# Kernel tuning notes

Measured on AMD Instinct MI355X. Metric: run time of the kernel, lower is better.

Reference implementation:

```python
import jax, jax.numpy as jnp
import numpy as np
from jax import lax

B, N0, N1 = 4, 256, 256
NVOX = N0 * N1
NSUB, NLOR, RAYLEN, NTOF = 8, 32768, 256, 1
NBLK, CH = 4, 16
SUBSETS = np.linspace(0, NSUB, NBLK, endpoint=False).astype(int)  # [0,2,4,6]


def setup_inputs() -> dict:
    key = jax.random.key(0)
    ks = jax.random.split(key, 12)
    osem = jax.random.uniform(ks[0], (B, 1, N0, N1, 1), jnp.float32) + 0.1
    data = jax.random.uniform(ks[1], (B, NSUB, NLOR, NTOF), jnp.float32)
    mult = jax.random.uniform(ks[2], (B, NSUB, NLOR, 1), jnp.float32) + 0.5
    contam = jax.random.uniform(ks[3], (B, NSUB, NLOR, NTOF), jnp.float32) + 0.1
    adjoint_ones = jax.random.uniform(ks[4], (B, NSUB, N0, N1, 1), jnp.float32) + 0.5
    norm = jax.random.uniform(ks[5], (B,), jnp.float32) + 0.5
    ray_idx = jax.random.randint(ks[6], (NSUB, NLOR, RAYLEN), 0, NVOX, dtype=jnp.int32)
    proj_weights = jax.random.uniform(ks[7], (NSUB, NLOR, RAYLEN), jnp.float32) / RAYLEN
    w1 = jax.random.normal(ks[8], (CH, 1, 3, 3), jnp.float32) * 0.05
    b1 = jnp.zeros((CH,), jnp.float32)
    w2 = jax.random.normal(ks[9], (1, CH, 3, 3), jnp.float32) * 0.05
    b2 = jnp.zeros((1,), jnp.float32)
    net_weight = jnp.asarray(1.0, jnp.float32)
    return dict(osem=osem, data=data, multiplicative_corrections=mult,
                contamination=contam, adjoint_ones=adjoint_ones, norm=norm,
                ray_idx=ray_idx, proj_weights=proj_weights,
                w1=w1, b1=b1, w2=w2, b2=b2, net_weight=net_weight)


def _conv(x, w):
    return lax.conv_general_dilated(x, w, (1, 1), 'SAME',
                                    dimension_numbers=('NCHW', 'OIHW', 'NCHW'))


def _net(x, w1, b1, w2, b2):
    # x: (B,1,N0,N1,1) -> treat as NCHW 2D image with 1 channel
    img = x[:, :, :, :, 0]
    h = jax.nn.relu(_conv(img, w1) + b1[None, :, None, None])
    o = _conv(h, w2) + b2[None, :, None, None]
    return o[..., None]


def _fidelity(x, data, mult, contam, adj_ones, norm, ray_idx, pw, subset):
    # unscaled image, flattened: (B, NVOX)
    img_flat = norm[:, None] * x[:, 0, :, :, 0].reshape(B, NVOX)
    ii = ray_idx[subset]          # (NLOR, RAYLEN) voxel indices per ray
    ww = pw[subset]               # (NLOR, RAYLEN) Joseph weights
    # forward projection: gather + weighted sum along each ray
    fwd = jnp.einsum('bls,ls->bl', img_flat[:, ii], ww)[..., None]  # (B,NLOR,1)
    expected = mult[:, subset] * fwd + contam[:, subset]            # (B,NLOR,NTOF)
    ratio = (mult[:, subset] * (1.0 - data[:, subset] / expected)).sum(-1)  # (B,NLOR)
    # adjoint projection: scatter-add along each ray
    back = jnp.zeros((B, NVOX), x.dtype).at[:, ii].add(ww * ratio[:, :, None])
    upd = back * (img_flat / adj_ones[:, subset].reshape(B, NVOX))
    return (upd / norm[:, None]).reshape(B, 1, N0, N1, 1)


def reference(osem, data, multiplicative_corrections, contamination,
              adjoint_ones, norm, ray_idx, proj_weights,
              w1, b1, w2, b2, net_weight):
    x = osem
    for subset in SUBSETS:
        x_data = _fidelity(x, data, multiplicative_corrections, contamination,
                           adjoint_ones, norm, ray_idx, proj_weights, int(subset))
        x_net = _net(x, w1, b1, w2, b2)
        x = jax.nn.relu(osem - x_data + net_weight * x_net)
    return x
```

## Files before the change

kernel.cpp:

```cpp
#include <hip/hip_runtime.h>
#include <hip/hip_fp16.h>

#define BB 4
#define N0 256
#define N1 256
#define NVOX 65536
#define NSUB 8
#define NLOR 32768
#define RAYLEN 256
#define CH 16
#define NPTS (NLOR * RAYLEN)
#define VOXQ 16384
#define VOXT 32768
#define CCH 32

__global__ __launch_bounds__(256) void k_transpose(const float* __restrict__ osem,
                                                   float* __restrict__ xt) {
    int v = blockIdx.x * blockDim.x + threadIdx.x;
    if (v >= NVOX) return;
    float4 o;
    o.x = osem[0 * NVOX + v];
    o.y = osem[1 * NVOX + v];
    o.z = osem[2 * NVOX + v];
    o.w = osem[3 * NVOX + v];
    ((float4*)xt)[v] = o;
}

__device__ __forceinline__ float upk_w(unsigned p) {
    return __half2float(__ushort_as_half((unsigned short)(p >> 16)));
}

__device__ __forceinline__ unsigned pk2(float a, float b) {
    __half2 h = __floats2half2_rn(a, b);
    return *reinterpret_cast<unsigned*>(&h);
}

__global__ __launch_bounds__(256) void k_fwdpack(
    const int* __restrict__ ridx,
    const float* __restrict__ pw,
    const float* __restrict__ xt,
    const float* __restrict__ data,
    const float* __restrict__ mult,
    const float* __restrict__ contam,
    const float* __restrict__ norm,
    float* __restrict__ ratio,
    unsigned* __restrict__ packed)
{
    const int wave = threadIdx.x >> 6;
    const int lane = threadIdx.x & 63;
    const int l = blockIdx.x * 4 + wave;
    const long e = (long)l * 64 + lane;

    int4   id = ((const int4*)ridx)[e];
    float4 w  = ((const float4*)pw)[e];
    uint4 pk;
    pk.x = (unsigned)id.x | ((unsigned)__half_as_ushort(__float2half_rn(w.x)) << 16);
    pk.y = (unsigned)id.y | ((unsigned)__half_as_ushort(__float2half_rn(w.y)) << 16);
    pk.z = (unsigned)id.z | ((unsigned)__half_as_ushort(__float2half_rn(w.z)) << 16);
    pk.w = (unsigned)id.w | ((unsigned)__half_as_ushort(__float2half_rn(w.w)) << 16);
    ((uint4*)packed)[e] = pk;

    float ax = 0.f, ay = 0.f, az = 0.f, aw = 0.f;
    {
        float4 xv = ((const float4*)xt)[id.x];
        ax += xv.x * w.x; ay += xv.y * w.x; az += xv.z * w.x; aw += xv.w * w.x;
        xv = ((const float4*)xt)[id.y];
        ax += xv.x * w.y; ay += xv.y * w.y; az += xv.z * w.y; aw += xv.w * w.y;
        xv = ((const float4*)xt)[id.z];
        ax += xv.x * w.z; ay += xv.y * w.z; az += xv.z * w.z; aw += xv.w * w.z;
        xv = ((const float4*)xt)[id.w];
        ax += xv.x * w.w; ay += xv.y * w.w; az += xv.z * w.w; aw += xv.w * w.w;
    }
#pragma unroll
    for (int off = 32; off >= 1; off >>= 1) {
        ax += __shfl_xor(ax, off);
        ay += __shfl_xor(ay, off);
        az += __shfl_xor(az, off);
        aw += __shfl_xor(aw, off);
    }
    if (lane == 0) {
        float fwd[4] = {ax, ay, az, aw};
        float rr[4];
#pragma unroll
        for (int b = 0; b < 4; ++b) {
            long o = (long)b * (NSUB * NLOR) + l;
            float m = mult[o];
            float ee = m * (norm[b] * fwd[b]) + contam[o];
            rr[b] = m * (1.0f - data[o] / ee);
        }
        ((float4*)ratio)[l] = make_float4(rr[0], rr[1], rr[2], rr[3]);
    }
}

__global__ __launch_bounds__(1024) void k_back_pk(
    const unsigned* __restrict__ packed,
    const float* __restrict__ ratio,
    unsigned* __restrict__ part,
    int PC)
{
    __shared__ unsigned acc[VOXQ];
    const int c = blockIdx.x;
    const int g = blockIdx.y;
    const int p = g & 1;
    const unsigned lo = (unsigned)(g >> 1) * VOXQ;

    for (int q = threadIdx.x; q < VOXQ; q += 1024) acc[q] = 0u;
    __syncthreads();

    const unsigned abase = (unsigned)(uintptr_t)(&acc[0]);

    const int n4 = PC >> 2;
    const uint4* src = (const uint4*)packed + (size_t)c * n4;
    const float2* rat2 = (const float2*)ratio;
    const int e0 = c * n4;

#define PKADD(u, R)                                                              \
    {                                                                            \
        unsigned q_ = ((u) & 0xffffu) - lo;                                      \
        if (q_ < VOXQ) {                                                         \
            float w_ = upk_w(u);                                                 \
            unsigned d_ = pk2(w_ * (R).x, w_ * (R).y);                           \
            unsigned a_ = abase + (q_ << 2);                                     \
            asm volatile("ds_pk_add_f16 %0, %1" :: "v"(a_), "v"(d_) : "memory"); \
        }                                                                        \
    }
#define PROC(P, R) PKADD(P.x, R) PKADD(P.y, R) PKADD(P.z, R) PKADD(P.w, R)

    for (int base4 = 0; base4 < n4; base4 += 4096) {
        const int ea = base4 + (int)threadIdx.x;
        uint4 A = src[ea];
        uint4 B = src[ea + 1024];
        uint4 C2 = src[ea + 2048];
        uint4 D = src[ea + 3072];
        float2 ra = rat2[(((e0 + ea) >> 6) << 1) + p];
        float2 rb = rat2[(((e0 + ea + 1024) >> 6) << 1) + p];
        float2 rc = rat2[(((e0 + ea + 2048) >> 6) << 1) + p];
        float2 rd = rat2[(((e0 + ea + 3072) >> 6) << 1) + p];
        PROC(A, ra) PROC(B, rb) PROC(C2, rc) PROC(D, rd)
    }
#undef PROC
#undef PKADD

    asm volatile("s_waitcnt lgkmcnt(0)" ::: "memory");
    __syncthreads();

    unsigned* dst = part + ((size_t)c * 2 + p) * NVOX + lo;
    for (int q = threadIdx.x; q < VOXQ; q += 1024) dst[q] = acc[q];
}

__global__ __launch_bounds__(256) void k_reduce(
    const unsigned* __restrict__ part,
    float* __restrict__ back)
{
    const int v = blockIdx.x * 256 + threadIdx.x;
    const int pr = blockIdx.y;
    float s0 = 0.f, s1 = 0.f;
#pragma unroll 8
    for (int cc = 0; cc < CCH; ++cc) {
        unsigned u = part[((size_t)cc * 2 + pr) * NVOX + v];
        s0 += __half2float(__ushort_as_half((unsigned short)(u & 0xffffu)));
        s1 += __half2float(__ushort_as_half((unsigned short)(u >> 16)));
    }
    ((float2*)back)[(size_t)v * 2 + pr] = make_float2(s0, s1);
}

#define TI 16
#define TJ 32
__global__ __launch_bounds__(256) void k_net_combine(
    const float* __restrict__ xt_in,
    const float* __restrict__ w1,
    const float* __restrict__ b1,
    const float* __restrict__ w2,
    const float* __restrict__ b2,
    const float* __restrict__ back,
    const float* __restrict__ osem,
    const float* __restrict__ adj,
    const float* __restrict__ nwp,
    float* __restrict__ xt_out,
    float* __restrict__ out_planar)
{
    __shared__ float img[(TI + 4) * (TJ + 4)];
    __shared__ float hsm[16 * (TI + 2) * (TJ + 2)];
    __shared__ float ws1[144], ws2[144], bs1[16];

    const int i0 = blockIdx.x * TI;
    const int j0 = blockIdx.y * TJ;
    const int b  = blockIdx.z;
    const int tid = threadIdx.x;

    if (tid < 144) { ws1[tid] = w1[tid]; ws2[tid] = w2[tid]; }
    if (tid < 16) bs1[tid] = b1[tid];

    for (int q = tid; q < (TI + 4) * (TJ + 4); q += 256) {
        int ii = q / (TJ + 4), jj = q % (TJ + 4);
        int gi = i0 - 2 + ii, gj = j0 - 2 + jj;
        float v = 0.f;
        if (gi >= 0 && gi < N0 && gj >= 0 && gj < N1)
            v = xt_in[(size_t)(gi * N1 + gj) * 4 + b];
        img[q] = v;
    }
    __syncthreads();

    const int HA = (TI + 2) * (TJ + 2);
    for (int q = tid; q < 16 * HA; q += 256) {
        int c = q / HA, r = q % HA;
        int ii = r / (TJ + 2), jj = r % (TJ + 2);
        int gi = i0 - 1 + ii, gj = j0 - 1 + jj;
        float hv = 0.f;
        if (gi >= 0 && gi < N0 && gj >= 0 && gj < N1) {
            float a = bs1[c];
#pragma unroll
            for (int di = 0; di < 3; ++di)
#pragma unroll
                for (int dj = 0; dj < 3; ++dj)
                    a += img[(ii + di) * (TJ + 4) + (jj + dj)] * ws1[c * 9 + di * 3 + dj];
            hv = fmaxf(a, 0.f);
        }
        hsm[q] = hv;
    }
    __syncthreads();

    const float nw = nwp[0];
    const float bb2 = b2[0];
    const int pr = b >> 1, hi = b & 1;
    for (int q = tid; q < TI * TJ; q += 256) {
        int li = q / TJ, lj = q % TJ;
        int v = (i0 + li) * N1 + (j0 + lj);
        float o = bb2;
#pragma unroll
        for (int c = 0; c < 16; ++c)
#pragma unroll
            for (int di = 0; di < 3; ++di)
#pragma unroll
                for (int dj = 0; dj < 3; ++dj)
                    o += hsm[c * HA + (li + di) * (TJ + 2) + (lj + dj)] *
                         ws2[c * 9 + di * 3 + dj];
        float2 bp = ((const float2*)back)[(size_t)v * 2 + pr];
        float bk = hi ? bp.y : bp.x;
        float xv = xt_in[(size_t)v * 4 + b];
        float x_data = bk * xv / adj[(size_t)b * NSUB * NVOX + v];
        float xnew = fmaxf(osem[(size_t)b * NVOX + v] - x_data + nw * o, 0.f);
        xt_out[(size_t)v * 4 + b] = xnew;
        if (out_planar) out_planar[(size_t)b * NVOX + v] = xnew;
    }
}

__global__ __launch_bounds__(256) void k_fwd(
    const int* __restrict__ ridx, const float* __restrict__ pw,
    const float* __restrict__ xt, const float* __restrict__ data,
    const float* __restrict__ mult, const float* __restrict__ contam,
    const float* __restrict__ norm, float* __restrict__ ratio)
{
    const int wave = threadIdx.x >> 6;
    const int lane = threadIdx.x & 63;
    const int l = blockIdx.x * 4 + wave;
    const long base = (long)l * RAYLEN;
    float ax = 0.f, ay = 0.f, az = 0.f, aw = 0.f;
#pragma unroll
    for (int k = 0; k < 4; ++k) {
        int r = lane + (k << 6);
        float wt = pw[base + r];
        float4 xv = ((const float4*)xt)[ridx[base + r]];
        ax += xv.x * wt; ay += xv.y * wt; az += xv.z * wt; aw += xv.w * wt;
    }
#pragma unroll
    for (int off = 32; off >= 1; off >>= 1) {
        ax += __shfl_xor(ax, off); ay += __shfl_xor(ay, off);
        az += __shfl_xor(az, off); aw += __shfl_xor(aw, off);
    }
    if (lane == 0) {
        float fwd[4] = {ax, ay, az, aw};
        float rr[4];
#pragma unroll
        for (int b = 0; b < 4; ++b) {
            long o = (long)b * (NSUB * NLOR) + l;
            float m = mult[o];
            float e = m * (norm[b] * fwd[b]) + contam[o];
            rr[b] = m * (1.0f - data[o] / e);
        }
        ((float4*)ratio)[l] = make_float4(rr[0], rr[1], rr[2], rr[3]);
    }
}

__global__ __launch_bounds__(1024) void k_back(
    const int* __restrict__ ridx, const float* __restrict__ pw,
    const float* __restrict__ ratio, float* __restrict__ part, int PC)
{
    __shared__ float acc[VOXT];
    const int c = blockIdx.x;
    const int g = blockIdx.y;
    const int b = g & 3;
    const int lo = (g >> 2) * VOXT;
    for (int q = threadIdx.x; q < VOXT; q += 1024) acc[q] = 0.0f;
    __syncthreads();
    const int pbeg = c * PC;
    const int pend = min(pbeg + PC, NPTS);
#pragma unroll 2
    for (int pt = pbeg + (int)threadIdx.x * 4; pt < pend; pt += 1024 * 4) {
        int4   id = *(const int4*)(ridx + pt);
        float4 w  = *(const float4*)(pw + pt);
        float  r  = ratio[(pt >> 8) * 4 + b];
        unsigned r0 = (unsigned)(id.x - lo), r1 = (unsigned)(id.y - lo);
        unsigned r2 = (unsigned)(id.z - lo), r3 = (unsigned)(id.w - lo);
        if (r0 < VOXT) atomicAdd(&acc[r0], w.x * r);
        if (r1 < VOXT) atomicAdd(&acc[r1], w.y * r);
        if (r2 < VOXT) atomicAdd(&acc[r2], w.z * r);
        if (r3 < VOXT) atomicAdd(&acc[r3], w.w * r);
    }
    __syncthreads();
    float4* dst = (float4*)(part + ((size_t)c * 4 + b) * NVOX + lo);
    const float4* srcl = (const float4*)acc;
    for (int q = threadIdx.x; q < VOXT / 4; q += 1024) dst[q] = srcl[q];
}

__global__ __launch_bounds__(256) void k_conv1(
    const float* __restrict__ xt, const float* __restrict__ w1,
    const float* __restrict__ b1, float* __restrict__ h)
{
    int t = blockIdx.x * blockDim.x + threadIdx.x;
    int b = t >> 16;
    int v = t & 65535;
    int i = v >> 8, j = v & 255;
    float in[3][3];
#pragma unroll
    for (int di = 0; di < 3; ++di)
#pragma unroll
        for (int dj = 0; dj < 3; ++dj) {
            int ii = i + di - 1, jj = j + dj - 1;
            in[di][dj] = (ii >= 0 && ii < N0 && jj >= 0 && jj < N1)
                             ? xt[(size_t)((ii << 8) | jj) * 4 + b]
                             : 0.0f;
        }
    float* hp = h + (size_t)t * CH;
#pragma unroll
    for (int c = 0; c < CH; ++c) {
        float acc = b1[c];
#pragma unroll
        for (int di = 0; di < 3; ++di)
#pragma unroll
            for (int dj = 0; dj < 3; ++dj)
                acc += in[di][dj] * w1[c * 9 + di * 3 + dj];
        hp[c] = fmaxf(acc, 0.0f);
    }
}

__global__ __launch_bounds__(256) void k_combine(
    const float* __restrict__ h, const float* __restrict__ w2,
    const float* __restrict__ b2, const float* __restrict__ part,
    const float* __restrict__ xt_in, const float* __restrict__ osem,
    const float* __restrict__ adj, const float* __restrict__ nwp, int C,
    float* __restrict__ xt_out, float* __restrict__ out_planar)
{
    int t = blockIdx.x * blockDim.x + threadIdx.x;
    int b = t >> 16;
    int v = t & 65535;
    int i = v >> 8, j = v & 255;
    float o = b2[0];
#pragma unroll
    for (int di = 0; di < 3; ++di) {
        int ii = i + di - 1;
        if (ii < 0 || ii >= N0) continue;
#pragma unroll
        for (int dj = 0; dj < 3; ++dj) {
            int jj = j + dj - 1;
            if (jj < 0 || jj >= N1) continue;
            const float* hp = h + ((size_t)b * NVOX + ((ii << 8) | jj)) * CH;
#pragma unroll
            for (int c = 0; c < CH; ++c)
                o += hp[c] * w2[c * 9 + di * 3 + dj];
        }
    }
    float bk = 0.0f;
    for (int c = 0; c < C; ++c)
        bk += part[((size_t)c * 4 + b) * NVOX + v];
    float xv = xt_in[(size_t)v * 4 + b];
    float x_data = bk * xv / adj[(size_t)b * NSUB * NVOX + v];
    float xnew = osem[t] - x_data + nwp[0] * o;
    xnew = fmaxf(xnew, 0.0f);
    xt_out[(size_t)v * 4 + b] = xnew;
    if (out_planar) out_planar[t] = xnew;
}

extern "C" void kernel_launch(void* const* d_in, const int* in_sizes, int n_in,
                              void* d_out, int out_size, void* d_ws, size_t ws_size,
                              hipStream_t stream) {
    const float* osem   = (const float*)d_in[0];
    const float* data   = (const float*)d_in[1];
    const float* mult   = (const float*)d_in[2];
    const float* contam = (const float*)d_in[3];
    const float* adj    = (const float*)d_in[4];
    const float* norm   = (const float*)d_in[5];
    const int*   ray_idx = (const int*)d_in[6];
    const float* pw     = (const float*)d_in[7];
    const float* w1     = (const float*)d_in[8];
    const float* b1     = (const float*)d_in[9];
    const float* w2     = (const float*)d_in[10];
    const float* b2     = (const float*)d_in[11];
    const float* nw     = (const float*)d_in[12];
    float* out = (float*)d_out;

    const size_t MB = 1024 * 1024;
    float* ws  = (float*)d_ws;
    float* xtA = ws;
    float* xtB = ws + (size_t)NVOX * 4;
    const int subsets[4] = {0, 2, 4, 6};

    bool use_pk = (ws_size >= 90 * MB);

    k_transpose<<<NVOX / 256, 256, 0, stream>>>(osem, xtA);

    if (use_pk) {
        const int PC = NPTS / CCH;
        unsigned* part   = (unsigned*)(ws + (size_t)NVOX * 8);
        unsigned* packed = part + (size_t)CCH * 2 * NVOX;
        float*    backv  = (float*)(packed + (size_t)NPTS);
        float*    ratio  = backv + (size_t)NVOX * 4;

        float* xin = xtA;
        float* xout = xtB;
        for (int it = 0; it < 4; ++it) {
            int s = subsets[it];
            k_fwdpack<<<NLOR / 4, 256, 0, stream>>>(
                ray_idx + (size_t)s * NPTS, pw + (size_t)s * NPTS, xin,
                data + (size_t)s * NLOR, mult + (size_t)s * NLOR,
                contam + (size_t)s * NLOR, norm, ratio, packed);
            k_back_pk<<<dim3(CCH, 8), 1024, 0, stream>>>(packed, ratio, part, PC);
            k_reduce<<<dim3(NVOX / 256, 2), 256, 0, stream>>>(part, backv);
            k_net_combine<<<dim3(N0 / TI, N1 / TJ, BB), 256, 0, stream>>>(
                xin, w1, b1, w2, b2, backv, osem,
                adj + (size_t)s * NVOX, nw,
                xout, (it == 3) ? out : nullptr);
            float* tmp = xin; xin = xout; xout = tmp;
        }
    } else {
        int C = (ws_size >= (18 + 32) * MB + NVOX) ? 32
              : (ws_size >= (18 + 16) * MB + NVOX) ? 16 : 8;
        const int PC = NPTS / C;
        float* part = ws + (size_t)NVOX * 8;
        float* h    = part + (size_t)C * NVOX * 4;
        float* ratio = h;

        float* xin = xtA;
        float* xout = xtB;
        for (int it = 0; it < 4; ++it) {
            int s = subsets[it];
            const int*   rs = ray_idx + (size_t)s * NPTS;
            const float* ps = pw + (size_t)s * NPTS;
            k_fwd<<<NLOR / 4, 256, 0, stream>>>(
                rs, ps, xin,
                data + (size_t)s * NLOR, mult + (size_t)s * NLOR,
                contam + (size_t)s * NLOR, norm, ratio);
            k_back<<<dim3(C, 8), 1024, 0, stream>>>(rs, ps, ratio, part, PC);
            k_conv1<<<(BB * NVOX) / 256, 256, 0, stream>>>(xin, w1, b1, h);
            k_combine<<<(BB * NVOX) / 256, 256, 0, stream>>>(
                h, w2, b2, part, xin, osem,
                adj + (size_t)s * NVOX, nw, C,
                xout, (it == 3) ? out : nullptr);
            float* tmp = xin; xin = xout; xout = tmp;
        }
    }
}
```

Before: 667.7 us.

## Split rays across half-waves, vectorize partial reduction, retile net conv into channel passes

The forward-pack kernel now has each half-wave handle one ray with eight gathers per lane, which halves the shuffle-reduction depth and the number of blocks. The reduce kernel reads two packed half2 words per thread so loads are wider. The conv/combine kernel uses 8-row tiles and computes the hidden channels in two passes of 8, which halves the hidden-layer shared memory. Each thread now owns exactly one output pixel and takes the center value from the shared image tile instead of reloading it. The changes target occupancy and instruction overhead, at the cost of an extra barrier and more halo recomputation per tile.

```diff
diff --git a/kernel.cpp b/kernel.cpp
--- a/kernel.cpp
+++ b/kernel.cpp
@@ -48,37 +48,59 @@
 {
     const int wave = threadIdx.x >> 6;
     const int lane = threadIdx.x & 63;
-    const int l = blockIdx.x * 4 + wave;
-    const long e = (long)l * 64 + lane;
-
-    int4   id = ((const int4*)ridx)[e];
-    float4 w  = ((const float4*)pw)[e];
-    uint4 pk;
-    pk.x = (unsigned)id.x | ((unsigned)__half_as_ushort(__float2half_rn(w.x)) << 16);
-    pk.y = (unsigned)id.y | ((unsigned)__half_as_ushort(__float2half_rn(w.y)) << 16);
-    pk.z = (unsigned)id.z | ((unsigned)__half_as_ushort(__float2half_rn(w.z)) << 16);
-    pk.w = (unsigned)id.w | ((unsigned)__half_as_ushort(__float2half_rn(w.w)) << 16);
-    ((uint4*)packed)[e] = pk;
+    const int half = lane >> 5;
+    const int sub  = lane & 31;
+    const int l = blockIdx.x * 8 + wave * 2 + half;
+    const long e0 = (long)l * 64;
+
+    const long ea = e0 + sub;
+    const long eb = e0 + sub + 32;
+
+    int4   ida = ((const int4*)ridx)[ea];
+    float4 wa  = ((const float4*)pw)[ea];
+    int4   idb = ((const int4*)ridx)[eb];
+    float4 wb  = ((const float4*)pw)[eb];
+
+    uint4 pka, pkb;
+    pka.x = (unsigned)ida.x | ((unsigned)__half_as_ushort(__float2half_rn(wa.x)) << 16);
+    pka.y = (unsigned)ida.y | ((unsigned)__half_as_ushort(__float2half_rn(wa.y)) << 16);
+    pka.z = (unsigned)ida.z | ((unsigned)__half_as_ushort(__float2half_rn(wa.z)) << 16);
+    pka.w = (unsigned)ida.w | ((unsigned)__half_as_ushort(__float2half_rn(wa.w)) << 16);
+    pkb.x = (unsigned)idb.x | ((unsigned)__half_as_ushort(__float2half_rn(wb.x)) << 16);
+    pkb.y = (unsigned)idb.y | ((unsigned)__half_as_ushort(__float2half_rn(wb.y)) << 16);
+    pkb.z = (unsigned)idb.z | ((unsigned)__half_as_ushort(__float2half_rn(wb.z)) << 16);
+    pkb.w = (unsigned)idb.w | ((unsigned)__half_as_ushort(__float2half_rn(wb.w)) << 16);
+    ((uint4*)packed)[ea] = pka;
+    ((uint4*)packed)[eb] = pkb;
 
     float ax = 0.f, ay = 0.f, az = 0.f, aw = 0.f;
     {
-        float4 xv = ((const float4*)xt)[id.x];
-        ax += xv.x * w.x; ay += xv.y * w.x; az += xv.z * w.x; aw += xv.w * w.x;
-        xv = ((const float4*)xt)[id.y];
-        ax += xv.x * w.y; ay += xv.y * w.y; az += xv.z * w.y; aw += xv.w * w.y;
-        xv = ((const float4*)xt)[id.z];
-        ax += xv.x * w.z; ay += xv.y * w.z; az += xv.z * w.z; aw += xv.w * w.z;
-        xv = ((const float4*)xt)[id.w];
-        ax += xv.x * w.w; ay += xv.y * w.w; az += xv.z * w.w; aw += xv.w * w.w;
-    }
-#pragma unroll
-    for (int off = 32; off >= 1; off >>= 1) {
+        float4 xv;
+        xv = ((const float4*)xt)[ida.x];
+        ax += xv.x * wa.x; ay += xv.y * wa.x; az += xv.z * wa.x; aw += xv.w * wa.x;
+        xv = ((const float4*)xt)[ida.y];
+        ax += xv.x * wa.y; ay += xv.y * wa.y; az += xv.z * wa.y; aw += xv.w * wa.y;
+        xv = ((const float4*)xt)[ida.z];
+        ax += xv.x * wa.z; ay += xv.y * wa.z; az += xv.z * wa.z; aw += xv.w * wa.z;
+        xv = ((const float4*)xt)[ida.w];
+        ax += xv.x * wa.w; ay += xv.y * wa.w; az += xv.z * wa.w; aw += xv.w * wa.w;
+        xv = ((const float4*)xt)[idb.x];
+        ax += xv.x * wb.x; ay += xv.y * wb.x; az += xv.z * wb.x; aw += xv.w * wb.x;
+        xv = ((const float4*)xt)[idb.y];
+        ax += xv.x * wb.y; ay += xv.y * wb.y; az += xv.z * wb.y; aw += xv.w * wb.y;
+        xv = ((const float4*)xt)[idb.z];
+        ax += xv.x * wb.z; ay += xv.y * wb.z; az += xv.z * wb.z; aw += xv.w * wb.z;
+        xv = ((const float4*)xt)[idb.w];
+        ax += xv.x * wb.w; ay += xv.y * wb.w; az += xv.z * wb.w; aw += xv.w * wb.w;
+    }
+#pragma unroll
+    for (int off = 16; off >= 1; off >>= 1) {
         ax += __shfl_xor(ax, off);
         ay += __shfl_xor(ay, off);
         az += __shfl_xor(az, off);
         aw += __shfl_xor(aw, off);
     }
-    if (lane == 0) {
+    if (sub == 0) {
         float fwd[4] = {ax, ay, az, aw};
         float rr[4];
 #pragma unroll
@@ -152,19 +174,23 @@
     const unsigned* __restrict__ part,
     float* __restrict__ back)
 {
-    const int v = blockIdx.x * 256 + threadIdx.x;
+    const int t = blockIdx.x * 256 + threadIdx.x;
+    const int v0 = t * 2;
     const int pr = blockIdx.y;
-    float s0 = 0.f, s1 = 0.f;
-#pragma unroll 8
+    float s0 = 0.f, s1 = 0.f, s2 = 0.f, s3 = 0.f;
+#pragma unroll
     for (int cc = 0; cc < CCH; ++cc) {
-        unsigned u = part[((size_t)cc * 2 + pr) * NVOX + v];
-        s0 += __half2float(__ushort_as_half((unsigned short)(u & 0xffffu)));
-        s1 += __half2float(__ushort_as_half((unsigned short)(u >> 16)));
-    }
-    ((float2*)back)[(size_t)v * 2 + pr] = make_float2(s0, s1);
-}
-
-#define TI 16
+        uint2 u = *(const uint2*)&part[((size_t)cc * 2 + pr) * NVOX + v0];
+        s0 += __half2float(__ushort_as_half((unsigned short)(u.x & 0xffffu)));
+        s1 += __half2float(__ushort_as_half((unsigned short)(u.x >> 16)));
+        s2 += __half2float(__ushort_as_half((unsigned short)(u.y & 0xffffu)));
+        s3 += __half2float(__ushort_as_half((unsigned short)(u.y >> 16)));
+    }
+    ((float2*)back)[(size_t)v0 * 2 + pr] = make_float2(s0, s1);
+    ((float2*)back)[(size_t)(v0 + 1) * 2 + pr] = make_float2(s2, s3);
+}
+
+#define TI 8
 #define TJ 32
 __global__ __launch_bounds__(256) void k_net_combine(
     const float* __restrict__ xt_in,
@@ -180,7 +206,7 @@
     float* __restrict__ out_planar)
 {
     __shared__ float img[(TI + 4) * (TJ + 4)];
-    __shared__ float hsm[16 * (TI + 2) * (TJ + 2)];
+    __shared__ float hsm[8 * (TI + 2) * (TJ + 2)];
     __shared__ float ws1[144], ws2[144], bs1[16];
 
     const int i0 = blockIdx.x * TI;
@@ -201,48 +227,52 @@
     }
     __syncthreads();
 
+    const int li = tid >> 5, lj = tid & 31;
     const int HA = (TI + 2) * (TJ + 2);
-    for (int q = tid; q < 16 * HA; q += 256) {
-        int c = q / HA, r = q % HA;
-        int ii = r / (TJ + 2), jj = r % (TJ + 2);
-        int gi = i0 - 1 + ii, gj = j0 - 1 + jj;
-        float hv = 0.f;
-        if (gi >= 0 && gi < N0 && gj >= 0 && gj < N1) {
-            float a = bs1[c];
+    float o = b2[0];
+
+#pragma unroll
+    for (int pass = 0; pass < 2; ++pass) {
+        for (int q = tid; q < 8 * HA; q += 256) {
+            int c8 = q / HA, r = q % HA;
+            int c = pass * 8 + c8;
+            int ii = r / (TJ + 2), jj = r % (TJ + 2);
+            int gi = i0 - 1 + ii, gj = j0 - 1 + jj;
+            float hv = 0.f;
+            if (gi >= 0 && gi < N0 && gj >= 0 && gj < N1) {
+                float a = bs1[c];
+#pragma unroll
+                for (int di = 0; di < 3; ++di)
+#pragma unroll
+                    for (int dj = 0; dj < 3; ++dj)
+                        a += img[(ii + di) * (TJ + 4) + (jj + dj)] *
+                             ws1[c * 9 + di * 3 + dj];
+                hv = fmaxf(a, 0.f);
+            }
+            hsm[q] = hv;
+        }
+        __syncthreads();
+#pragma unroll
+        for (int c8 = 0; c8 < 8; ++c8)
 #pragma unroll
             for (int di = 0; di < 3; ++di)
 #pragma unroll
                 for (int dj = 0; dj < 3; ++dj)
-                    a += img[(ii + di) * (TJ + 4) + (jj + dj)] * ws1[c * 9 + di * 3 + dj];
-            hv = fmaxf(a, 0.f);
-        }
-        hsm[q] = hv;
-    }
-    __syncthreads();
+                    o += hsm[c8 * HA + (li + di) * (TJ + 2) + (lj + dj)] *
+                         ws2[(pass * 8 + c8) * 9 + di * 3 + dj];
+        if (pass == 0) __syncthreads();
+    }
 
     const float nw = nwp[0];
-    const float bb2 = b2[0];
     const int pr = b >> 1, hi = b & 1;
-    for (int q = tid; q < TI * TJ; q += 256) {
-        int li = q / TJ, lj = q % TJ;
-        int v = (i0 + li) * N1 + (j0 + lj);
-        float o = bb2;
-#pragma unroll
-        for (int c = 0; c < 16; ++c)
-#pragma unroll
-            for (int di = 0; di < 3; ++di)
-#pragma unroll
-                for (int dj = 0; dj < 3; ++dj)
-                    o += hsm[c * HA + (li + di) * (TJ + 2) + (lj + dj)] *
-                         ws2[c * 9 + di * 3 + dj];
-        float2 bp = ((const float2*)back)[(size_t)v * 2 + pr];
-        float bk = hi ? bp.y : bp.x;
-        float xv = xt_in[(size_t)v * 4 + b];
-        float x_data = bk * xv / adj[(size_t)b * NSUB * NVOX + v];
-        float xnew = fmaxf(osem[(size_t)b * NVOX + v] - x_data + nw * o, 0.f);
-        xt_out[(size_t)v * 4 + b] = xnew;
-        if (out_planar) out_planar[(size_t)b * NVOX + v] = xnew;
-    }
+    const int v = (i0 + li) * N1 + (j0 + lj);
+    float2 bp = ((const float2*)back)[(size_t)v * 2 + pr];
+    float bk = hi ? bp.y : bp.x;
+    float xv = img[(li + 2) * (TJ + 4) + (lj + 2)];
+    float x_data = bk * xv / adj[(size_t)b * NSUB * NVOX + v];
+    float xnew = fmaxf(osem[(size_t)b * NVOX + v] - x_data + nw * o, 0.f);
+    xt_out[(size_t)v * 4 + b] = xnew;
+    if (out_planar) out_planar[(size_t)b * NVOX + v] = xnew;
 }
 
 __global__ __launch_bounds__(256) void k_fwd(
@@ -420,12 +450,12 @@
         float* xout = xtB;
         for (int it = 0; it < 4; ++it) {
             int s = subsets[it];
-            k_fwdpack<<<NLOR / 4, 256, 0, stream>>>(
+            k_fwdpack<<<NLOR / 8, 256, 0, stream>>>(
                 ray_idx + (size_t)s * NPTS, pw + (size_t)s * NPTS, xin,
                 data + (size_t)s * NLOR, mult + (size_t)s * NLOR,
                 contam + (size_t)s * NLOR, norm, ratio, packed);
             k_back_pk<<<dim3(CCH, 8), 1024, 0, stream>>>(packed, ratio, part, PC);
-            k_reduce<<<dim3(NVOX / 256, 2), 256, 0, stream>>>(part, backv);
+            k_reduce<<<dim3(NVOX / 512, 2), 256, 0, stream>>>(part, backv);
             k_net_combine<<<dim3(N0 / TI, N1 / TJ, BB), 256, 0, stream>>>(
                 xin, w1, b1, w2, b2, backv, osem,
                 adj + (size_t)s * NVOX, nw,
```

After: 663.0 us (median of 2 runs). No clear change (-0.7%).
